# Kernel optimization log

Measured on AMD Instinct MI355X. Metric: run time of the kernel, lower is better.

Reference implementation:

```python
import jax, jax.numpy as jnp
import numpy as np

V = 1_000_000
NODE_DIM = 128
HIDDEN = 128
OUT_DIM = 128
GLOBAL_DIM = 64
N_GRAPH = 50_000


def setup_inputs() -> dict:
    key = jax.random.key(0)
    ks = jax.random.split(key, 10)
    s1 = 1.0 / np.sqrt(NODE_DIM)
    s3 = 1.0 / np.sqrt(2 * HIDDEN + GLOBAL_DIM)
    return {
        "x": jax.random.normal(ks[0], (V, NODE_DIM), dtype=jnp.float32),
        "node2graph": jax.random.randint(ks[1], (V,), 0, N_GRAPH, dtype=jnp.int64),
        "global_x": jax.random.normal(ks[2], (N_GRAPH, GLOBAL_DIM), dtype=jnp.float32),
        "W1": jax.random.uniform(ks[3], (HIDDEN, NODE_DIM), jnp.float32, -s1, s1),
        "b1": jax.random.uniform(ks[4], (HIDDEN,), jnp.float32, -s1, s1),
        "W2": jax.random.uniform(ks[5], (HIDDEN, NODE_DIM), jnp.float32, -s1, s1),
        "b2": jax.random.uniform(ks[6], (HIDDEN,), jnp.float32, -s1, s1),
        "W3": jax.random.uniform(ks[7], (OUT_DIM, 2 * HIDDEN + GLOBAL_DIM), jnp.float32, -s3, s3),
        "b3": jax.random.uniform(ks[8], (OUT_DIM,), jnp.float32, -s3, s3),
    }


def reference(x, node2graph, global_x, W1, b1, W2, b2, W3, b3):
    # gated projection: linear1(x) * sigmoid(linear2(x))   [V, H]
    h = (x @ W1.T + b1) * jax.nn.sigmoid(x @ W2.T + b2)
    # segment sum / mean over graphs   [N, H]
    Z1 = jax.ops.segment_sum(h, node2graph, num_segments=N_GRAPH)
    counts = jax.ops.segment_sum(jnp.ones((h.shape[0],), h.dtype), node2graph,
                                 num_segments=N_GRAPH)
    Z2 = Z1 / jnp.maximum(counts, 1.0)[:, None]
    Z = jnp.concatenate([Z1, Z2, global_x], axis=-1)  # [N, 2H+Fg]
    return jax.nn.relu(Z @ W3.T + b3)  # [N, OUT_DIM]
```

## Files before the change

### kernel.cpp

```cpp
#include <hip/hip_runtime.h>
#include <cmath>

#define V_NODES  1000000
#define NODE_DIM 128
#define HIDDEN   128
#define OUT_DIM  128
#define GDIM     64
#define NGRAPH   50000

typedef unsigned short u16;
typedef __attribute__((ext_vector_type(8))) short          short8;
typedef __attribute__((ext_vector_type(8))) unsigned short ushort8;
typedef __attribute__((ext_vector_type(8))) __bf16         bf16x8;
typedef __attribute__((ext_vector_type(4))) float          f32x4;

__device__ __forceinline__ u16 f2bf(float f) {
  unsigned u = __builtin_bit_cast(unsigned, f);
  u += 0x7fff + ((u >> 16) & 1);
  return (u16)(u >> 16);
}

__device__ __forceinline__ f32x4 mfma_bf16(bf16x8 a, bf16x8 b, f32x4 c) {
  return __builtin_amdgcn_mfma_f32_16x16x32_bf16(a, b, c, 0, 0, 0);
}

__global__ __launch_bounds__(256) void convert_weights(
    const float* __restrict__ W1, const float* __restrict__ W2,
    const float* __restrict__ W3,
    u16* __restrict__ w1b, u16* __restrict__ w2b, u16* __restrict__ w3b) {
  int i = blockIdx.x * 256 + threadIdx.x;
  if (i < NODE_DIM * HIDDEN) {
    w1b[i] = f2bf(W1[i]);
    w2b[i] = f2bf(W2[i]);
  }
  if (i < OUT_DIM * (2 * HIDDEN + GDIM)) w3b[i] = f2bf(W3[i]);
}

__global__ __launch_bounds__(256, 2) void gated_scatter(
    const float* __restrict__ x, const int* __restrict__ n2g,
    const u16* __restrict__ w1b, const u16* __restrict__ w2b,
    const float* __restrict__ b1, const float* __restrict__ b2,
    float* __restrict__ Z1, float* __restrict__ cnt) {
  extern __shared__ u16 lds[];
  u16* sW1 = lds;
  u16* sW2 = lds + 16384;
  const int tid = threadIdx.x;

#pragma unroll
  for (int i = 0; i < 8; ++i) {
    int m = i * 256 + tid;
    int n = m >> 4, c = m & 15;
    int p = c ^ (n & 15);
    *(ushort8*)(sW1 + n * 128 + p * 8) = *(const ushort8*)(w1b + m * 8);
    *(ushort8*)(sW2 + n * 128 + p * 8) = *(const ushort8*)(w2b + m * 8);
  }
  __syncthreads();

  const int lane = tid & 63;
  const int wv   = tid >> 6;
  const int q    = lane >> 4;
  const int mr   = lane & 15;
  const int rowbase = blockIdx.x * 64 + wv * 16;
  const int arow    = rowbase + mr;

  f32x4 acc1[8] = {};
  f32x4 acc2[8] = {};

#pragma unroll
  for (int kc = 0; kc < 4; ++kc) {
    const int k0 = kc * 32;
    const float* ap = x + (size_t)arow * NODE_DIM + k0 + q * 8;
    float4 a0 = *(const float4*)ap;
    float4 a1 = *(const float4*)(ap + 4);
    bf16x8 af;
    af[0] = (__bf16)a0.x; af[1] = (__bf16)a0.y; af[2] = (__bf16)a0.z; af[3] = (__bf16)a0.w;
    af[4] = (__bf16)a1.x; af[5] = (__bf16)a1.y; af[6] = (__bf16)a1.z; af[7] = (__bf16)a1.w;

    const int p = ((k0 >> 3) + q) ^ mr;
#pragma unroll
    for (int t = 0; t < 8; ++t) {
      const int n = t * 16 + mr;
      short8 bs1 = *(const short8*)(sW1 + n * 128 + p * 8);
      short8 bs2 = *(const short8*)(sW2 + n * 128 + p * 8);
      acc1[t] = mfma_bf16(af, __builtin_bit_cast(bf16x8, bs1), acc1[t]);
      acc2[t] = mfma_bf16(af, __builtin_bit_cast(bf16x8, bs2), acc2[t]);
    }
  }

  int g[4];
#pragma unroll
  for (int r = 0; r < 4; ++r) g[r] = n2g[rowbase + q * 4 + r];

#pragma unroll
  for (int t = 0; t < 8; ++t) {
    const int col = t * 16 + mr;
    const float bb1 = b1[col];
    const float bb2 = b2[col];
#pragma unroll
    for (int r = 0; r < 4; ++r) {
      float l1 = acc1[t][r] + bb1;
      float l2 = acc2[t][r] + bb2;
      float h  = l1 / (1.0f + __expf(-l2));
      atomicAdd(Z1 + (size_t)g[r] * HIDDEN + col, h);
    }
  }

  if (tid < 64) atomicAdd(cnt + n2g[blockIdx.x * 64 + tid], 1.0f);
}

__global__ __launch_bounds__(256, 4) void readout_k(
    const float* __restrict__ Z1, const float* __restrict__ cnt,
    const float* __restrict__ gx, const u16* __restrict__ w3b,
    const float* __restrict__ b3, float* __restrict__ out) {
  const int tid  = threadIdx.x;
  const int lane = tid & 63;
  const int wv   = tid >> 6;
  const int q    = lane >> 4;
  const int mr   = lane & 15;
  const int rowbase = blockIdx.x * 64 + wv * 16;
  const int arow    = rowbase + mr;
  const bool rowok  = arow < NGRAPH;

  float inv = 0.0f;
  if (rowok) inv = 1.0f / fmaxf(cnt[arow], 1.0f);

  f32x4 acc[8] = {};

#pragma unroll
  for (int kc = 0; kc < 10; ++kc) {
    const int k0 = kc * 32;
    float av[8];
    if (rowok) {
      if (k0 < 128) {
        const float* p = Z1 + (size_t)arow * HIDDEN + k0 + q * 8;
        float4 a0 = *(const float4*)p;
        float4 a1 = *(const float4*)(p + 4);
        av[0]=a0.x; av[1]=a0.y; av[2]=a0.z; av[3]=a0.w;
        av[4]=a1.x; av[5]=a1.y; av[6]=a1.z; av[7]=a1.w;
      } else if (k0 < 256) {
        const float* p = Z1 + (size_t)arow * HIDDEN + (k0 - 128) + q * 8;
        float4 a0 = *(const float4*)p;
        float4 a1 = *(const float4*)(p + 4);
        av[0]=a0.x*inv; av[1]=a0.y*inv; av[2]=a0.z*inv; av[3]=a0.w*inv;
        av[4]=a1.x*inv; av[5]=a1.y*inv; av[6]=a1.z*inv; av[7]=a1.w*inv;
      } else {
        const float* p = gx + (size_t)arow * GDIM + (k0 - 256) + q * 8;
        float4 a0 = *(const float4*)p;
        float4 a1 = *(const float4*)(p + 4);
        av[0]=a0.x; av[1]=a0.y; av[2]=a0.z; av[3]=a0.w;
        av[4]=a1.x; av[5]=a1.y; av[6]=a1.z; av[7]=a1.w;
      }
    } else {
#pragma unroll
      for (int j = 0; j < 8; ++j) av[j] = 0.0f;
    }
    bf16x8 af;
#pragma unroll
    for (int j = 0; j < 8; ++j) af[j] = (__bf16)av[j];

#pragma unroll
    for (int t = 0; t < 8; ++t) {
      const int n = t * 16 + mr;
      short8 bs = *(const short8*)(w3b + (size_t)n * (2 * HIDDEN + GDIM) + k0 + q * 8);
      acc[t] = mfma_bf16(af, __builtin_bit_cast(bf16x8, bs), acc[t]);
    }
  }

#pragma unroll
  for (int t = 0; t < 8; ++t) {
    const int col = t * 16 + mr;
    const float bb = b3[col];
#pragma unroll
    for (int r = 0; r < 4; ++r) {
      const int row = rowbase + q * 4 + r;
      if (row < NGRAPH)
        out[(size_t)row * OUT_DIM + col] = fmaxf(acc[t][r] + bb, 0.0f);
    }
  }
}

extern "C" void kernel_launch(void* const* d_in, const int* in_sizes, int n_in,
                              void* d_out, int out_size, void* d_ws, size_t ws_size,
                              hipStream_t stream) {
  const float* x   = (const float*)d_in[0];
  const int*   n2g = (const int*)d_in[1];
  const float* gx  = (const float*)d_in[2];
  const float* W1  = (const float*)d_in[3];
  const float* b1  = (const float*)d_in[4];
  const float* W2  = (const float*)d_in[5];
  const float* b2  = (const float*)d_in[6];
  const float* W3  = (const float*)d_in[7];
  const float* b3  = (const float*)d_in[8];
  float* out = (float*)d_out;

  char* ws = (char*)d_ws;
  u16*   w1b = (u16*)(ws);
  u16*   w2b = (u16*)(ws + 32768);
  u16*   w3b = (u16*)(ws + 65536);
  float* Z1  = (float*)(ws + 147456);
  float* cnt = (float*)(ws + 147456 + (size_t)NGRAPH * HIDDEN * 4);

  hipMemsetAsync(ws + 147456, 0,
                 (size_t)NGRAPH * HIDDEN * 4 + (size_t)NGRAPH * 4, stream);

  convert_weights<<<160, 256, 0, stream>>>(W1, W2, W3, w1b, w2b, w3b);

  gated_scatter<<<V_NODES / 64, 256, 2 * 16384 * sizeof(u16), stream>>>(
      x, n2g, w1b, w2b, b1, b2, Z1, cnt);

  readout_k<<<(NGRAPH + 63) / 64, 256, 0, stream>>>(Z1, cnt, gx, w3b, b3, out);
}
```

Measured before the change: 1.076 ms.

## Replace atomic scatter with counting-sort and per-graph gather reduction

Replaces the float atomicAdd scatter of gated node features into per-graph sums with a counting sort of nodes by graph (histogram, scan, rank), a compute kernel that writes the gated features as bf16, and a gather kernel where each wavefront sums the nodes of one graph. The aim is to remove 128M float atomics and the large memset of Z1. In exchange it adds several kernels, a single-block scan, 256MB of bf16 intermediate traffic, random row gathers, and bf16 rounding of h before summation. The old path is kept as a fallback when the workspace is too small.

```diff
diff --git a/kernel.cpp b/kernel.cpp
--- a/kernel.cpp
+++ b/kernel.cpp
@@ -9,13 +9,14 @@
 #define NGRAPH   50000
 
 typedef unsigned short u16;
+typedef unsigned int   u32;
 typedef __attribute__((ext_vector_type(8))) short          short8;
 typedef __attribute__((ext_vector_type(8))) unsigned short ushort8;
 typedef __attribute__((ext_vector_type(8))) __bf16         bf16x8;
 typedef __attribute__((ext_vector_type(4))) float          f32x4;
 
 __device__ __forceinline__ u16 f2bf(float f) {
-  unsigned u = __builtin_bit_cast(unsigned, f);
+  u32 u = __builtin_bit_cast(u32, f);
   u += 0x7fff + ((u >> 16) & 1);
   return (u16)(u >> 16);
 }
@@ -34,6 +35,144 @@
     w2b[i] = f2bf(W2[i]);
   }
   if (i < OUT_DIM * (2 * HIDDEN + GDIM)) w3b[i] = f2bf(W3[i]);
+}
+
+__global__ __launch_bounds__(256) void hist_k(const int* __restrict__ n2g,
+                                              int* __restrict__ hist) {
+  int i = blockIdx.x * 256 + threadIdx.x;
+  if (i < V_NODES) atomicAdd(hist + n2g[i], 1);
+}
+
+#define CHUNK 49
+__global__ __launch_bounds__(1024) void scan_k(const int* __restrict__ hist,
+                                               int* __restrict__ offsets,
+                                               int* __restrict__ cursor) {
+  __shared__ int part[1024];
+  const int tid = threadIdx.x;
+  const int beg = tid * CHUNK;
+  const int end = min(beg + CHUNK, NGRAPH);
+  int val = 0;
+  for (int i = beg; i < end; ++i) val += hist[i];
+  part[tid] = val;
+  __syncthreads();
+  for (int off = 1; off < 1024; off <<= 1) {
+    int v = (tid >= off) ? part[tid - off] : 0;
+    __syncthreads();
+    part[tid] += v;
+    __syncthreads();
+  }
+  int run = part[tid] - val;
+  for (int i = beg; i < end; ++i) {
+    offsets[i] = run;
+    cursor[i]  = run;
+    run += hist[i];
+  }
+  if (beg < NGRAPH && NGRAPH <= beg + CHUNK) offsets[NGRAPH] = run;
+}
+
+__global__ __launch_bounds__(256) void rank_k(const int* __restrict__ n2g,
+                                              int* __restrict__ cursor,
+                                              int* __restrict__ order) {
+  int i = blockIdx.x * 256 + threadIdx.x;
+  if (i < V_NODES) {
+    int g = n2g[i];
+    int p = atomicAdd(cursor + g, 1);
+    order[p] = i;
+  }
+}
+
+__global__ __launch_bounds__(256, 2) void gated_compute(
+    const float* __restrict__ x,
+    const u16* __restrict__ w1b, const u16* __restrict__ w2b,
+    const float* __restrict__ b1, const float* __restrict__ b2,
+    u16* __restrict__ hs) {
+  extern __shared__ u16 lds[];
+  u16* sW1 = lds;
+  u16* sW2 = lds + 16384;
+  const int tid = threadIdx.x;
+
+#pragma unroll
+  for (int i = 0; i < 8; ++i) {
+    int m = i * 256 + tid;
+    int n = m >> 4, c = m & 15;
+    int p = c ^ (n & 15);
+    *(ushort8*)(sW1 + n * 128 + p * 8) = *(const ushort8*)(w1b + m * 8);
+    *(ushort8*)(sW2 + n * 128 + p * 8) = *(const ushort8*)(w2b + m * 8);
+  }
+  __syncthreads();
+
+  const int lane = tid & 63;
+  const int wv   = tid >> 6;
+  const int q    = lane >> 4;
+  const int mr   = lane & 15;
+  const int rowbase = blockIdx.x * 64 + wv * 16;
+  const int arow    = rowbase + mr;
+
+  f32x4 acc1[8] = {};
+  f32x4 acc2[8] = {};
+
+#pragma unroll
+  for (int kc = 0; kc < 4; ++kc) {
+    const int k0 = kc * 32;
+    const float* ap = x + (size_t)arow * NODE_DIM + k0 + q * 8;
+    float4 a0 = *(const float4*)ap;
+    float4 a1 = *(const float4*)(ap + 4);
+    bf16x8 af;
+    af[0] = (__bf16)a0.x; af[1] = (__bf16)a0.y; af[2] = (__bf16)a0.z; af[3] = (__bf16)a0.w;
+    af[4] = (__bf16)a1.x; af[5] = (__bf16)a1.y; af[6] = (__bf16)a1.z; af[7] = (__bf16)a1.w;
+
+    const int p = ((k0 >> 3) + q) ^ mr;
+#pragma unroll
+    for (int t = 0; t < 8; ++t) {
+      const int n = t * 16 + mr;
+      short8 bs1 = *(const short8*)(sW1 + n * 128 + p * 8);
+      short8 bs2 = *(const short8*)(sW2 + n * 128 + p * 8);
+      acc1[t] = mfma_bf16(af, __builtin_bit_cast(bf16x8, bs1), acc1[t]);
+      acc2[t] = mfma_bf16(af, __builtin_bit_cast(bf16x8, bs2), acc2[t]);
+    }
+  }
+
+#pragma unroll
+  for (int t = 0; t < 8; ++t) {
+    const int col = t * 16 + mr;
+    const float bb1 = b1[col];
+    const float bb2 = b2[col];
+#pragma unroll
+    for (int r = 0; r < 4; ++r) {
+      float l1 = acc1[t][r] + bb1;
+      float l2 = acc2[t][r] + bb2;
+      float h  = l1 / (1.0f + __expf(-l2));
+      hs[(size_t)(rowbase + q * 4 + r) * HIDDEN + col] = f2bf(h);
+    }
+  }
+}
+
+__global__ __launch_bounds__(256) void gather_sum(
+    const u16* __restrict__ hs, const int* __restrict__ offsets,
+    const int* __restrict__ order,
+    float* __restrict__ Z1, float* __restrict__ cnt) {
+  const int tid  = threadIdx.x;
+  const int lane = tid & 63;
+  const int wv   = tid >> 6;
+  const int g    = blockIdx.x * 4 + wv;
+
+  const int beg = offsets[g];
+  const int end = offsets[g + 1];
+
+  float ax = 0.0f, ay = 0.0f;
+  for (int base = beg; base < end; base += 64) {
+    int idx = 0;
+    if (base + lane < end) idx = order[base + lane];
+    const int m = min(64, end - base);
+    for (int j = 0; j < m; ++j) {
+      int node = __shfl(idx, j);
+      u32 pk = ((const u32*)(hs + (size_t)node * HIDDEN))[lane];
+      ax += __builtin_bit_cast(float, pk << 16);
+      ay += __builtin_bit_cast(float, pk & 0xFFFF0000u);
+    }
+  }
+  ((float2*)(Z1 + (size_t)g * HIDDEN))[lane] = make_float2(ax, ay);
+  if (lane == 0) cnt[g] = (float)(end - beg);
 }
 
 __global__ __launch_bounds__(256, 2) void gated_scatter(
@@ -45,7 +184,6 @@
   u16* sW1 = lds;
   u16* sW2 = lds + 16384;
   const int tid = threadIdx.x;
-
 #pragma unroll
   for (int i = 0; i < 8; ++i) {
     int m = i * 256 + tid;
@@ -55,17 +193,14 @@
     *(ushort8*)(sW2 + n * 128 + p * 8) = *(const ushort8*)(w2b + m * 8);
   }
   __syncthreads();
-
   const int lane = tid & 63;
   const int wv   = tid >> 6;
   const int q    = lane >> 4;
   const int mr   = lane & 15;
   const int rowbase = blockIdx.x * 64 + wv * 16;
   const int arow    = rowbase + mr;
-
   f32x4 acc1[8] = {};
   f32x4 acc2[8] = {};
-
 #pragma unroll
   for (int kc = 0; kc < 4; ++kc) {
     const int k0 = kc * 32;
@@ -75,7 +210,6 @@
     bf16x8 af;
     af[0] = (__bf16)a0.x; af[1] = (__bf16)a0.y; af[2] = (__bf16)a0.z; af[3] = (__bf16)a0.w;
     af[4] = (__bf16)a1.x; af[5] = (__bf16)a1.y; af[6] = (__bf16)a1.z; af[7] = (__bf16)a1.w;
-
     const int p = ((k0 >> 3) + q) ^ mr;
 #pragma unroll
     for (int t = 0; t < 8; ++t) {
@@ -86,11 +220,9 @@
       acc2[t] = mfma_bf16(af, __builtin_bit_cast(bf16x8, bs2), acc2[t]);
     }
   }
-
   int g[4];
 #pragma unroll
   for (int r = 0; r < 4; ++r) g[r] = n2g[rowbase + q * 4 + r];
-
 #pragma unroll
   for (int t = 0; t < 8; ++t) {
     const int col = t * 16 + mr;
@@ -104,7 +236,6 @@
       atomicAdd(Z1 + (size_t)g[r] * HIDDEN + col, h);
     }
   }
-
   if (tid < 64) atomicAdd(cnt + n2g[blockIdx.x * 64 + tid], 1.0f);
 }
 
@@ -194,19 +325,48 @@
   float* out = (float*)d_out;
 
   char* ws = (char*)d_ws;
-  u16*   w1b = (u16*)(ws);
-  u16*   w2b = (u16*)(ws + 32768);
-  u16*   w3b = (u16*)(ws + 65536);
-  float* Z1  = (float*)(ws + 147456);
-  float* cnt = (float*)(ws + 147456 + (size_t)NGRAPH * HIDDEN * 4);
-
-  hipMemsetAsync(ws + 147456, 0,
-                 (size_t)NGRAPH * HIDDEN * 4 + (size_t)NGRAPH * 4, stream);
+  const size_t oW1   = 0;
+  const size_t oW2   = 32768;
+  const size_t oW3   = 65536;
+  const size_t oHist = 147456;
+  const size_t oOffs = oHist + (size_t)NGRAPH * 4;
+  const size_t oCur  = oOffs + ((size_t)NGRAPH + 1) * 4;
+  const size_t oOrd  = oCur  + (size_t)NGRAPH * 4;
+  const size_t oZ1   = (oOrd + (size_t)V_NODES * 4 + 255) & ~(size_t)255;
+  const size_t oCnt  = oZ1 + (size_t)NGRAPH * HIDDEN * 4;
+  const size_t oH    = (oCnt + (size_t)NGRAPH * 4 + 255) & ~(size_t)255;
+  const size_t NEED  = oH + (size_t)V_NODES * HIDDEN * 2;
+
+  u16*   w1b = (u16*)(ws + oW1);
+  u16*   w2b = (u16*)(ws + oW2);
+  u16*   w3b = (u16*)(ws + oW3);
+  float* Z1  = (float*)(ws + oZ1);
+  float* cnt = (float*)(ws + oCnt);
 
   convert_weights<<<160, 256, 0, stream>>>(W1, W2, W3, w1b, w2b, w3b);
 
-  gated_scatter<<<V_NODES / 64, 256, 2 * 16384 * sizeof(u16), stream>>>(
-      x, n2g, w1b, w2b, b1, b2, Z1, cnt);
+  if (ws_size >= NEED) {
+    int*   hist    = (int*)(ws + oHist);
+    int*   offsets = (int*)(ws + oOffs);
+    int*   cursor  = (int*)(ws + oCur);
+    int*   order   = (int*)(ws + oOrd);
+    u16*   hsbuf   = (u16*)(ws + oH);
+
+    hipMemsetAsync(hist, 0, (size_t)NGRAPH * 4, stream);
+    hist_k<<<(V_NODES + 255) / 256, 256, 0, stream>>>(n2g, hist);
+    scan_k<<<1, 1024, 0, stream>>>(hist, offsets, cursor);
+    rank_k<<<(V_NODES + 255) / 256, 256, 0, stream>>>(n2g, cursor, order);
+
+    gated_compute<<<V_NODES / 64, 256, 2 * 16384 * sizeof(u16), stream>>>(
+        x, w1b, w2b, b1, b2, hsbuf);
+
+    gather_sum<<<NGRAPH / 4, 256, 0, stream>>>(hsbuf, offsets, order, Z1, cnt);
+  } else {
+    hipMemsetAsync(ws + oZ1, 0, (size_t)NGRAPH * HIDDEN * 4 + (size_t)NGRAPH * 4,
+                   stream);
+    gated_scatter<<<V_NODES / 64, 256, 2 * 16384 * sizeof(u16), stream>>>(
+        x, n2g, w1b, w2b, b1, b2, Z1, cnt);
+  }
 
   readout_k<<<(NGRAPH + 63) / 64, 256, 0, stream>>>(Z1, cnt, gx, w3b, b3, out);
 }
```

After: 1.173 ms. 1.09x slower.
